# Kernel optimization log

Hardware: AMD Instinct MI355X
Metric: run time of the kernel (lower is better)

## Reference

```python
import jax, jax.numpy as jnp
import numpy as np

N = 50000  # num nodes


def _gcn_layer(x, W, b, src, dst, dinv):
    # PyG GCNConv: transform first, then normalized neighbor aggregation
    h = x @ W                                   # [N, out]
    norm = dinv[src] * dinv[dst]                # [E]
    msg = h[src] * norm[:, None]                # gather + scale, [E, out]
    agg = jax.ops.segment_sum(msg, dst, num_segments=N)
    agg = agg + h * (dinv * dinv)[:, None]      # self-loop term (weight 1)
    return agg + b


def setup_inputs() -> dict:
    key = jax.random.key(0)
    ks = jax.random.split(key, 9)
    x = jax.random.normal(ks[0], (N, 256), dtype=jnp.float32)
    edge_index = jax.random.randint(ks[1], (2, 800000), 0, N, dtype=jnp.int64)
    def lin(kw, kb, fan_in, fan_out):
        s = 1.0 / np.sqrt(fan_in)
        W = jax.random.uniform(kw, (fan_in, fan_out), jnp.float32, -s, s)
        b = jax.random.uniform(kb, (fan_out,), jnp.float32, -s, s)
        return W, b
    W0, b0 = lin(ks[2], ks[3], 256, 128)
    W1, b1 = lin(ks[4], ks[5], 128, 128)
    W2, b2 = lin(ks[6], ks[7], 128, 64)
    return {"x": x, "edge_index": edge_index,
            "W0": W0, "b0": b0, "W1": W1, "b1": b1, "W2": W2, "b2": b2}


def reference(x, edge_index, W0, b0, W1, b1, W2, b2):
    src, dst = edge_index[0], edge_index[1]
    # degree with implicit self loops (edge weights = 1)
    deg = jax.ops.segment_sum(jnp.ones_like(dst, dtype=x.dtype), dst,
                              num_segments=N) + 1.0
    dinv = jax.lax.rsqrt(deg)
    h = jax.nn.relu(_gcn_layer(x, W0, b0, src, dst, dinv))
    h = jax.nn.relu(_gcn_layer(h, W1, b1, src, dst, dinv))
    out = _gcn_layer(h, W2, b2, src, dst, dinv)  # no relu on final layer
    return out
```

## Files before the change

kernel.cpp:

```cpp
#include <hip/hip_runtime.h>

#define NNODES 50000
#define NEDGES 800000
#define CHUNK 3125

typedef __attribute__((ext_vector_type(8))) short short8;
typedef __attribute__((ext_vector_type(4))) float floatx4;
typedef __attribute__((ext_vector_type(8))) _Float16 f16x8;

__device__ __forceinline__ void async16(const void* g, void* l) {
    __builtin_amdgcn_global_load_lds(
        (const __attribute__((address_space(1))) unsigned int*)g,
        (__attribute__((address_space(3))) unsigned int*)l, 16, 0, 0);
}

__device__ __forceinline__ void split_bf16(float v, short& hi, short& lo) {
    unsigned u = __float_as_uint(v);
    unsigned hu = u & 0xffff0000u;
    hi = (short)(hu >> 16);
    float r = v - __uint_as_float(hu);
    lo = (short)(__float_as_uint(r) >> 16);
}


__global__ void k_wprep3(const float* __restrict__ W0, short* __restrict__ W0h,
                         short* __restrict__ W0l, const float* __restrict__ W1,
                         short* __restrict__ W1h, short* __restrict__ W1l,
                         const float* __restrict__ W2, short* __restrict__ W2h,
                         short* __restrict__ W2l) {
    int id = blockIdx.x * 256 + threadIdx.x;
    const float* W; short *Wh, *Wl; int K, F;
    if (id < 32768) { W = W0; Wh = W0h; Wl = W0l; K = 256; F = 128; }
    else if (id < 49152) { id -= 32768; W = W1; Wh = W1h; Wl = W1l; K = 128; F = 128; }
    else if (id < 57344) { id -= 49152; W = W2; Wh = W2h; Wl = W2l; K = 128; F = 64; }
    else return;
    int f = id / K, k = id - f * K;
    short h, l;
    split_bf16(W[(size_t)k * F + f], h, l);
    Wh[id] = h;
    Wl[id] = l;
}

__global__ void k_split(const float* __restrict__ x, short* __restrict__ xh,
                        short* __restrict__ xl, int* __restrict__ chist, int n8) {
    int i = blockIdx.x * 256 + threadIdx.x;
    if (i < 256) chist[i] = 0;
    if (i >= n8) return;
    float4 v0 = ((const float4*)x)[i * 2];
    float4 v1 = ((const float4*)x)[i * 2 + 1];
    float va[8] = {v0.x, v0.y, v0.z, v0.w, v1.x, v1.y, v1.z, v1.w};
    short8 h8, l8;
#pragma unroll
    for (int j = 0; j < 8; j++) {
        short h, l;
        split_bf16(va[j], h, l);
        h8[j] = h; l8[j] = l;
    }
    *(short8*)&xh[i * 8] = h8;
    *(short8*)&xl[i * 8] = l8;
}


__global__ __launch_bounds__(256) void k_p1(const int* __restrict__ dst,
                                            int* __restrict__ chist) {
    __shared__ int h[256];
    int t = threadIdx.x, b = blockIdx.x;
    h[t] = 0;
    __syncthreads();
    int e0 = b * CHUNK;
#pragma unroll
    for (int k = 0; k < 13; k++) {
        int o = k * 256 + t;
        if (o < CHUNK) atomicAdd(&h[dst[e0 + o] >> 8], 1);
    }
    __syncthreads();
    if (h[t]) atomicAdd(&chist[t], h[t]);
}

__global__ void k_cscan(const int* __restrict__ chist, int* __restrict__ coff,
                        int* __restrict__ ccur, int* __restrict__ rowptr) {
    __shared__ int s[256];
    int t = threadIdx.x;
    int v = chist[t];
    s[t] = v; __syncthreads();
    for (int o = 1; o < 256; o <<= 1) {
        int x = (t >= o) ? s[t - o] : 0;
        __syncthreads();
        s[t] += x;
        __syncthreads();
    }
    int excl = s[t] - v;
    coff[t] = excl;
    ccur[t] = excl;
    if (t == 0) rowptr[NNODES] = NEDGES;
}

__global__ __launch_bounds__(256) void k_p2(const int* __restrict__ src,
                                            const int* __restrict__ dst,
                                            int* ccur, unsigned* __restrict__ buck) {
    __shared__ int hist[256];
    __shared__ int base[256];
    int t = threadIdx.x, b = blockIdx.x;
    hist[t] = 0;
    __syncthreads();
    int e0 = b * CHUNK;
    int myb[13]; int myi[13]; unsigned pk[13];
#pragma unroll
    for (int k = 0; k < 13; k++) {
        int o = k * 256 + t;
        if (o < CHUNK) {
            int s = src[e0 + o], d = dst[e0 + o];
            int bin = d >> 8;
            myb[k] = bin;
            myi[k] = atomicAdd(&hist[bin], 1);
            pk[k] = (unsigned)s | ((unsigned)(d & 255) << 16);
        }
    }
    __syncthreads();
    base[t] = hist[t] ? atomicAdd(&ccur[t], hist[t]) : 0;
    __syncthreads();
#pragma unroll
    for (int k = 0; k < 13; k++) {
        int o = k * 256 + t;
        if (o < CHUNK) buck[base[myb[k]] + myi[k]] = pk[k];
    }
}

__global__ __launch_bounds__(256) void k_p3(const unsigned* __restrict__ buck,
                                            const int* __restrict__ coff,
                                            const int* __restrict__ chist,
                                            int* __restrict__ rowptr,
                                            float* __restrict__ dinv,
                                            int* __restrict__ ssrc) {
    __shared__ int h[256], ex[256], cur[256];
    int t = threadIdx.x, b = blockIdx.x;
    int s0 = coff[b], S = chist[b];
    h[t] = 0;
    __syncthreads();
    for (int i = t; i < S; i += 256)
        atomicAdd(&h[(buck[s0 + i] >> 16) & 255], 1);
    __syncthreads();
    int v = h[t];
    ex[t] = v; __syncthreads();
    for (int o = 1; o < 256; o <<= 1) {
        int x = (t >= o) ? ex[t - o] : 0;
        __syncthreads();
        ex[t] += x;
        __syncthreads();
    }
    int excl = ex[t] - v;
    int n = b * 256 + t;
    if (n < NNODES) {
        rowptr[n] = s0 + excl;
        dinv[n] = rsqrtf((float)v + 1.0f);
    }
    cur[t] = excl;
    __syncthreads();
    for (int i = t; i < S; i += 256) {
        unsigned pk = buck[s0 + i];
        int dl = (pk >> 16) & 255;
        int p = atomicAdd(&cur[dl], 1);
        ssrc[s0 + p] = (int)(pk & 0xFFFFu);
    }
}


template <int BN>
__global__ __launch_bounds__(256) void k_gemm2(
    const short* __restrict__ Ah, const short* __restrict__ Al,
    const short* __restrict__ Bh, const short* __restrict__ Bl,
    const float* __restrict__ dinv, _Float16* __restrict__ g16,
    int M, int K) {
    constexpr int BM = 64, BK = 64;
    constexpr int NT = BN / 16;
    __shared__ __align__(16) short sAh[BM * BK], sAl[BM * BK];
    __shared__ __align__(16) short sBh[BN * BK], sBl[BN * BK];

    const int tid = threadIdx.x, lane = tid & 63, w = tid >> 6;
    const int row0 = blockIdx.x * BM;
    const int lr = lane >> 3;
    const int lz = lane & 7;
    const int swz = (lz ^ lr) * 8;
    const int fr = lane & 15, fq = lane >> 4;

    floatx4 acc[NT] = {};

    for (int k0 = 0; k0 < K; k0 += BK) {
#pragma unroll
        for (int jj = 0; jj < 2; jj++) {
            int j = w * 2 + jj;
            int grow = row0 + j * 8 + lr;
            if (grow >= M) grow = M - 1;
            size_t go = (size_t)grow * K + k0 + swz;
            async16(&Ah[go], &sAh[j * 8 * BK + lane * 8]);
            async16(&Al[go], &sAl[j * 8 * BK + lane * 8]);
        }
#pragma unroll
        for (int jj = 0; jj < BN / 32; jj++) {
            int j = w * (BN / 32) + jj;
            size_t go = (size_t)(j * 8 + lr) * K + k0 + swz;
            async16(&Bh[go], &sBh[j * 8 * BK + lane * 8]);
            async16(&Bl[go], &sBl[j * 8 * BK + lane * 8]);
        }
        __syncthreads();

#pragma unroll
        for (int ks = 0; ks < 2; ks++) {
            int R = w * 16 + fr;
            int ca = ((ks * 4 + fq) ^ (R & 7)) * 8;
            short8 ah = *(const short8*)&sAh[R * BK + ca];
            short8 al = *(const short8*)&sAl[R * BK + ca];
#pragma unroll
            for (int nt = 0; nt < NT; nt++) {
                int n = nt * 16 + fr;
                int cb = ((ks * 4 + fq) ^ (n & 7)) * 8;
                short8 bh = *(const short8*)&sBh[n * BK + cb];
                short8 bl = *(const short8*)&sBl[n * BK + cb];
                acc[nt] = __builtin_amdgcn_mfma_f32_16x16x32_bf16(ah, bh, acc[nt], 0, 0, 0);
                acc[nt] = __builtin_amdgcn_mfma_f32_16x16x32_bf16(ah, bl, acc[nt], 0, 0, 0);
                acc[nt] = __builtin_amdgcn_mfma_f32_16x16x32_bf16(al, bh, acc[nt], 0, 0, 0);
            }
        }
        __syncthreads();
    }

#pragma unroll
    for (int rr = 0; rr < 4; rr++) {
        int grow = row0 + w * 16 + fq * 4 + rr;
        if (grow < M) {
            float dv = dinv[grow];
#pragma unroll
            for (int nt = 0; nt < NT; nt++)
                g16[(size_t)grow * BN + nt * 16 + fr] =
                    (_Float16)(acc[nt][rr] * dv);
        }
    }
}


__global__ __launch_bounds__(256) void k_agg(const _Float16* __restrict__ g,
                                             const int* __restrict__ ssrc,
                                             const int* __restrict__ rowptr,
                                             const float* __restrict__ dinv,
                                             const float* __restrict__ bias,
                                             float* __restrict__ outf,
                                             short* __restrict__ oh,
                                             short* __restrict__ ol,
                                             int F, int lgF8, int relu, int writebf) {
    int gid = blockIdx.x * 256 + threadIdx.x;
    int F8 = F >> 3;
    int n = gid >> lgF8;
    if (n >= NNODES) return;
    int c8 = gid & (F8 - 1);
    const f16x8* gp = (const f16x8*)g;

    f16x8 sv = gp[(size_t)n * F8 + c8];
    float a0[8], a1[8], a2[8], a3[8];
#pragma unroll
    for (int j = 0; j < 8; j++) {
        a0[j] = (float)sv[j];
        a1[j] = 0.f; a2[j] = 0.f; a3[j] = 0.f;
    }
    int e0 = rowptr[n], e1 = rowptr[n + 1];
    int e = e0;
    for (; e + 4 <= e1; e += 4) {
        int s0 = ssrc[e], s1 = ssrc[e + 1], s2 = ssrc[e + 2], s3 = ssrc[e + 3];
        f16x8 v0 = gp[(size_t)s0 * F8 + c8];
        f16x8 v1 = gp[(size_t)s1 * F8 + c8];
        f16x8 v2 = gp[(size_t)s2 * F8 + c8];
        f16x8 v3 = gp[(size_t)s3 * F8 + c8];
#pragma unroll
        for (int j = 0; j < 8; j++) {
            a0[j] += (float)v0[j];
            a1[j] += (float)v1[j];
            a2[j] += (float)v2[j];
            a3[j] += (float)v3[j];
        }
    }
    for (; e < e1; e++) {
        int s = ssrc[e];
        f16x8 v = gp[(size_t)s * F8 + c8];
#pragma unroll
        for (int j = 0; j < 8; j++) a0[j] += (float)v[j];
    }
    float dv = dinv[n];
    float o[8];
#pragma unroll
    for (int j = 0; j < 8; j++) {
        float s = (a0[j] + a1[j]) + (a2[j] + a3[j]);
        o[j] = s * dv + bias[c8 * 8 + j];
        if (relu) o[j] = fmaxf(o[j], 0.f);
    }
    if (writebf) {
        short8 h8, l8;
#pragma unroll
        for (int j = 0; j < 8; j++) {
            short h, l;
            split_bf16(o[j], h, l);
            h8[j] = h; l8[j] = l;
        }
        *(short8*)&oh[(size_t)n * F + c8 * 8] = h8;
        *(short8*)&ol[(size_t)n * F + c8 * 8] = l8;
    } else {
        *(float4*)&outf[(size_t)n * F + c8 * 8] =
            make_float4(o[0], o[1], o[2], o[3]);
        *(float4*)&outf[(size_t)n * F + c8 * 8 + 4] =
            make_float4(o[4], o[5], o[6], o[7]);
    }
}


static inline size_t align256(size_t x) { return (x + 255) & ~(size_t)255; }

extern "C" void kernel_launch(void* const* d_in, const int* in_sizes, int n_in,
                              void* d_out, int out_size, void* d_ws, size_t ws_size,
                              hipStream_t stream) {
    const float* x  = (const float*)d_in[0];
    const int*   ei = (const int*)d_in[1];
    const float* W0 = (const float*)d_in[2];
    const float* b0 = (const float*)d_in[3];
    const float* W1 = (const float*)d_in[4];
    const float* b1 = (const float*)d_in[5];
    const float* W2 = (const float*)d_in[6];
    const float* b2 = (const float*)d_in[7];
    float* out = (float*)d_out;

    const int* src = ei;
    const int* dst = ei + NEDGES;

    char* w = (char*)d_ws;
    size_t off = 0;
    float* dinv   = (float*)(w + off); off = align256(off + NNODES * 4);
    int* rowptr   = (int*)(w + off);   off = align256(off + (NNODES + 1) * 4);
    int* chist    = (int*)(w + off);   off = align256(off + 256 * 4);
    int* coff     = (int*)(w + off);   off = align256(off + 256 * 4);
    int* ccur     = (int*)(w + off);   off = align256(off + 256 * 4);
    unsigned* buck = (unsigned*)(w + off); off = align256(off + (size_t)NEDGES * 4);
    int* ssrc     = (int*)(w + off);   off = align256(off + (size_t)NEDGES * 4);
    short* W0h    = (short*)(w + off); off = align256(off + 256 * 128 * 2);
    short* W0l    = (short*)(w + off); off = align256(off + 256 * 128 * 2);
    short* W1h    = (short*)(w + off); off = align256(off + 128 * 128 * 2);
    short* W1l    = (short*)(w + off); off = align256(off + 128 * 128 * 2);
    short* W2h    = (short*)(w + off); off = align256(off + 128 * 64 * 2);
    short* W2l    = (short*)(w + off); off = align256(off + 128 * 64 * 2);
    short* xh     = (short*)(w + off); off = align256(off + (size_t)NNODES * 256 * 2);
    short* xl     = (short*)(w + off); off = align256(off + (size_t)NNODES * 256 * 2);
    short* ph     = (short*)(w + off); off = align256(off + (size_t)NNODES * 128 * 2);
    short* pl     = (short*)(w + off); off = align256(off + (size_t)NNODES * 128 * 2);
    _Float16* g16 = (_Float16*)(w + off); off = align256(off + (size_t)NNODES * 128 * 2);

    k_wprep3<<<224, 256, 0, stream>>>(W0, W0h, W0l, W1, W1h, W1l, W2, W2h, W2l);
    k_split<<<(NNODES * 32 + 255) / 256, 256, 0, stream>>>(x, xh, xl, chist,
                                                           NNODES * 32);
    k_p1<<<256, 256, 0, stream>>>(dst, chist);
    k_cscan<<<1, 256, 0, stream>>>(chist, coff, ccur, rowptr);
    k_p2<<<256, 256, 0, stream>>>(src, dst, ccur, buck);
    k_p3<<<256, 256, 0, stream>>>(buck, coff, chist, rowptr, dinv, ssrc);

    const int MB = (NNODES + 63) / 64;

    k_gemm2<128><<<MB, 256, 0, stream>>>(xh, xl, W0h, W0l, dinv, g16, NNODES, 256);
    k_agg<<<(NNODES * 16 + 255) / 256, 256, 0, stream>>>(g16, ssrc, rowptr, dinv, b0,
                                                         (float*)nullptr, ph, pl,
                                                         128, 4, 1, 1);
    k_gemm2<128><<<MB, 256, 0, stream>>>(ph, pl, W1h, W1l, dinv, g16, NNODES, 128);
    k_agg<<<(NNODES * 16 + 255) / 256, 256, 0, stream>>>(g16, ssrc, rowptr, dinv, b1,
                                                         (float*)nullptr, ph, pl,
                                                         128, 4, 1, 1);
    k_gemm2<64><<<MB, 256, 0, stream>>>(ph, pl, W2h, W2l, dinv, g16, NNODES, 128);
    k_agg<<<(NNODES * 8 + 255) / 256, 256, 0, stream>>>(g16, ssrc, rowptr, dinv, b2,
                                                        out, (short*)nullptr,
                                                        (short*)nullptr, 64, 3, 0, 0);
    (void)in_sizes; (void)n_in; (void)out_size; (void)ws_size;
}
```

Baseline: 277.2 us.

## Merge prep kernels and give each node a full wavefront for aggregation

The weight split, input split and dst histogram kernels become one launch. Each histogram block writes its own row, and the scan kernel sums those rows, replacing the global atomics and the chist zeroing. Aggregation now gives one 64-lane wavefront to each node: lanes split the edges and combine their partial sums with xor shuffles. This spreads the gather more evenly across lanes, though with about 16 edges per node many lanes sit idle, and the shuffle reduction adds overhead.

```diff
diff --git a/kernel.cpp b/kernel.cpp
--- a/kernel.cpp
+++ b/kernel.cpp
@@ -23,65 +23,69 @@
 }
 
 
-__global__ void k_wprep3(const float* __restrict__ W0, short* __restrict__ W0h,
-                         short* __restrict__ W0l, const float* __restrict__ W1,
-                         short* __restrict__ W1h, short* __restrict__ W1l,
-                         const float* __restrict__ W2, short* __restrict__ W2h,
-                         short* __restrict__ W2l) {
-    int id = blockIdx.x * 256 + threadIdx.x;
-    const float* W; short *Wh, *Wl; int K, F;
-    if (id < 32768) { W = W0; Wh = W0h; Wl = W0l; K = 256; F = 128; }
-    else if (id < 49152) { id -= 32768; W = W1; Wh = W1h; Wl = W1l; K = 128; F = 128; }
-    else if (id < 57344) { id -= 49152; W = W2; Wh = W2h; Wl = W2l; K = 128; F = 64; }
-    else return;
-    int f = id / K, k = id - f * K;
-    short h, l;
-    split_bf16(W[(size_t)k * F + f], h, l);
-    Wh[id] = h;
-    Wl[id] = l;
-}
-
-__global__ void k_split(const float* __restrict__ x, short* __restrict__ xh,
-                        short* __restrict__ xl, int* __restrict__ chist, int n8) {
-    int i = blockIdx.x * 256 + threadIdx.x;
-    if (i < 256) chist[i] = 0;
-    if (i >= n8) return;
-    float4 v0 = ((const float4*)x)[i * 2];
-    float4 v1 = ((const float4*)x)[i * 2 + 1];
-    float va[8] = {v0.x, v0.y, v0.z, v0.w, v1.x, v1.y, v1.z, v1.w};
-    short8 h8, l8;
-#pragma unroll
-    for (int j = 0; j < 8; j++) {
+#define PREP_WBLK 224
+#define PREP_SBLK 6250
+#define PREP_TOT  (PREP_WBLK + PREP_SBLK + 256)
+
+__global__ __launch_bounds__(256) void k_prep(
+    const float* __restrict__ W0, short* __restrict__ W0h, short* __restrict__ W0l,
+    const float* __restrict__ W1, short* __restrict__ W1h, short* __restrict__ W1l,
+    const float* __restrict__ W2, short* __restrict__ W2h, short* __restrict__ W2l,
+    const float* __restrict__ x, short* __restrict__ xh, short* __restrict__ xl,
+    const int* __restrict__ dst, int* __restrict__ hist2d) {
+    int b = blockIdx.x, t = threadIdx.x;
+    if (b < PREP_WBLK) {
+        int id = b * 256 + t;
+        const float* W; short *Wh, *Wl; int K;
+        if (id < 32768) { W = W0; Wh = W0h; Wl = W0l; K = 256; }
+        else if (id < 49152) { id -= 32768; W = W1; Wh = W1h; Wl = W1l; K = 128; }
+        else if (id < 57344) { id -= 49152; W = W2; Wh = W2h; Wl = W2l; K = 128; }
+        else return;
+        int F = (W == W2) ? 64 : 128;
+        int f = id / K, k = id - f * K;
         short h, l;
-        split_bf16(va[j], h, l);
-        h8[j] = h; l8[j] = l;
-    }
-    *(short8*)&xh[i * 8] = h8;
-    *(short8*)&xl[i * 8] = l8;
-}
-
-
-__global__ __launch_bounds__(256) void k_p1(const int* __restrict__ dst,
-                                            int* __restrict__ chist) {
-    __shared__ int h[256];
-    int t = threadIdx.x, b = blockIdx.x;
-    h[t] = 0;
-    __syncthreads();
-    int e0 = b * CHUNK;
-#pragma unroll
-    for (int k = 0; k < 13; k++) {
-        int o = k * 256 + t;
-        if (o < CHUNK) atomicAdd(&h[dst[e0 + o] >> 8], 1);
-    }
-    __syncthreads();
-    if (h[t]) atomicAdd(&chist[t], h[t]);
-}
-
-__global__ void k_cscan(const int* __restrict__ chist, int* __restrict__ coff,
-                        int* __restrict__ ccur, int* __restrict__ rowptr) {
+        split_bf16(W[(size_t)k * F + f], h, l);
+        Wh[id] = h;
+        Wl[id] = l;
+    } else if (b < PREP_WBLK + PREP_SBLK) {
+        int i = (b - PREP_WBLK) * 256 + t;
+        float4 v0 = ((const float4*)x)[i * 2];
+        float4 v1 = ((const float4*)x)[i * 2 + 1];
+        float va[8] = {v0.x, v0.y, v0.z, v0.w, v1.x, v1.y, v1.z, v1.w};
+        short8 h8, l8;
+#pragma unroll
+        for (int j = 0; j < 8; j++) {
+            short h, l;
+            split_bf16(va[j], h, l);
+            h8[j] = h; l8[j] = l;
+        }
+        *(short8*)&xh[i * 8] = h8;
+        *(short8*)&xl[i * 8] = l8;
+    } else {
+        __shared__ int h[256];
+        int bb = b - PREP_WBLK - PREP_SBLK;
+        h[t] = 0;
+        __syncthreads();
+        int e0 = bb * CHUNK;
+#pragma unroll
+        for (int k = 0; k < 13; k++) {
+            int o = k * 256 + t;
+            if (o < CHUNK) atomicAdd(&h[dst[e0 + o] >> 8], 1);
+        }
+        __syncthreads();
+        hist2d[bb * 256 + t] = h[t];
+    }
+}
+
+__global__ void k_cscan(const int* __restrict__ hist2d, int* __restrict__ chist,
+                        int* __restrict__ coff, int* __restrict__ ccur,
+                        int* __restrict__ rowptr) {
     __shared__ int s[256];
     int t = threadIdx.x;
-    int v = chist[t];
+    int v = 0;
+#pragma unroll 8
+    for (int b = 0; b < 256; b++) v += hist2d[b * 256 + t];
+    chist[t] = v;
     s[t] = v; __syncthreads();
     for (int o = 1; o < 256; o <<= 1) {
         int x = (t >= o) ? s[t - o] : 0;
@@ -238,74 +242,77 @@
 }
 
 
-__global__ __launch_bounds__(256) void k_agg(const _Float16* __restrict__ g,
-                                             const int* __restrict__ ssrc,
-                                             const int* __restrict__ rowptr,
-                                             const float* __restrict__ dinv,
-                                             const float* __restrict__ bias,
-                                             float* __restrict__ outf,
-                                             short* __restrict__ oh,
-                                             short* __restrict__ ol,
-                                             int F, int lgF8, int relu, int writebf) {
-    int gid = blockIdx.x * 256 + threadIdx.x;
-    int F8 = F >> 3;
-    int n = gid >> lgF8;
-    if (n >= NNODES) return;
-    int c8 = gid & (F8 - 1);
+template <int F>
+__global__ __launch_bounds__(256) void k_aggw(const _Float16* __restrict__ g,
+                                              const int* __restrict__ ssrc,
+                                              const int* __restrict__ rowptr,
+                                              const float* __restrict__ dinv,
+                                              const float* __restrict__ bias,
+                                              float* __restrict__ outf,
+                                              short* __restrict__ oh,
+                                              short* __restrict__ ol,
+                                              int relu, int writebf) {
+    constexpr int C = F / 8;
+    constexpr int S = 64 / C;
+    int wid = (blockIdx.x * 256 + threadIdx.x) >> 6;
+    if (wid >= NNODES) return;
+    int lane = threadIdx.x & 63;
+    int c = lane & (C - 1);
+    int s = lane / C;
+    int n = wid;
     const f16x8* gp = (const f16x8*)g;
 
-    f16x8 sv = gp[(size_t)n * F8 + c8];
-    float a0[8], a1[8], a2[8], a3[8];
-#pragma unroll
-    for (int j = 0; j < 8; j++) {
-        a0[j] = (float)sv[j];
-        a1[j] = 0.f; a2[j] = 0.f; a3[j] = 0.f;
-    }
+    float acc[8];
+    if (s == 0) {
+        f16x8 v = gp[(size_t)n * C + c];
+#pragma unroll
+        for (int j = 0; j < 8; j++) acc[j] = (float)v[j];
+    } else {
+#pragma unroll
+        for (int j = 0; j < 8; j++) acc[j] = 0.f;
+    }
+
     int e0 = rowptr[n], e1 = rowptr[n + 1];
-    int e = e0;
-    for (; e + 4 <= e1; e += 4) {
-        int s0 = ssrc[e], s1 = ssrc[e + 1], s2 = ssrc[e + 2], s3 = ssrc[e + 3];
-        f16x8 v0 = gp[(size_t)s0 * F8 + c8];
-        f16x8 v1 = gp[(size_t)s1 * F8 + c8];
-        f16x8 v2 = gp[(size_t)s2 * F8 + c8];
-        f16x8 v3 = gp[(size_t)s3 * F8 + c8];
+    for (int e = e0 + s; e < e1; e += S) {
+        int sn = ssrc[e];
+        f16x8 v = gp[(size_t)sn * C + c];
+#pragma unroll
+        for (int j = 0; j < 8; j++) acc[j] += (float)v[j];
+    }
+
+#pragma unroll
+    for (int m = C; m < 64; m <<= 1) {
+#pragma unroll
+        for (int j = 0; j < 8; j++) acc[j] += __shfl_xor(acc[j], m, 64);
+    }
+
+    if (s == 0) {
+        float dv = dinv[n];
+        float4 bv0 = *(const float4*)&bias[c * 8];
+        float4 bv1 = *(const float4*)&bias[c * 8 + 4];
+        float bb[8] = {bv0.x, bv0.y, bv0.z, bv0.w, bv1.x, bv1.y, bv1.z, bv1.w};
+        float o[8];
 #pragma unroll
         for (int j = 0; j < 8; j++) {
-            a0[j] += (float)v0[j];
-            a1[j] += (float)v1[j];
-            a2[j] += (float)v2[j];
-            a3[j] += (float)v3[j];
-        }
-    }
-    for (; e < e1; e++) {
-        int s = ssrc[e];
-        f16x8 v = gp[(size_t)s * F8 + c8];
-#pragma unroll
-        for (int j = 0; j < 8; j++) a0[j] += (float)v[j];
-    }
-    float dv = dinv[n];
-    float o[8];
-#pragma unroll
-    for (int j = 0; j < 8; j++) {
-        float s = (a0[j] + a1[j]) + (a2[j] + a3[j]);
-        o[j] = s * dv + bias[c8 * 8 + j];
-        if (relu) o[j] = fmaxf(o[j], 0.f);
-    }
-    if (writebf) {
-        short8 h8, l8;
-#pragma unroll
-        for (int j = 0; j < 8; j++) {
-            short h, l;
-            split_bf16(o[j], h, l);
-            h8[j] = h; l8[j] = l;
-        }
-        *(short8*)&oh[(size_t)n * F + c8 * 8] = h8;
-        *(short8*)&ol[(size_t)n * F + c8 * 8] = l8;
-    } else {
-        *(float4*)&outf[(size_t)n * F + c8 * 8] =
-            make_float4(o[0], o[1], o[2], o[3]);
-        *(float4*)&outf[(size_t)n * F + c8 * 8 + 4] =
-            make_float4(o[4], o[5], o[6], o[7]);
+            o[j] = acc[j] * dv + bb[j];
+            if (relu) o[j] = fmaxf(o[j], 0.f);
+        }
+        if (writebf) {
+            short8 h8, l8;
+#pragma unroll
+            for (int j = 0; j < 8; j++) {
+                short h, l;
+                split_bf16(o[j], h, l);
+                h8[j] = h; l8[j] = l;
+            }
+            *(short8*)&oh[(size_t)n * F + c * 8] = h8;
+            *(short8*)&ol[(size_t)n * F + c * 8] = l8;
+        } else {
+            *(float4*)&outf[(size_t)n * F + c * 8] =
+                make_float4(o[0], o[1], o[2], o[3]);
+            *(float4*)&outf[(size_t)n * F + c * 8 + 4] =
+                make_float4(o[4], o[5], o[6], o[7]);
+        }
     }
 }
 
@@ -330,46 +337,43 @@
 
     char* w = (char*)d_ws;
     size_t off = 0;
-    float* dinv   = (float*)(w + off); off = align256(off + NNODES * 4);
-    int* rowptr   = (int*)(w + off);   off = align256(off + (NNODES + 1) * 4);
-    int* chist    = (int*)(w + off);   off = align256(off + 256 * 4);
-    int* coff     = (int*)(w + off);   off = align256(off + 256 * 4);
-    int* ccur     = (int*)(w + off);   off = align256(off + 256 * 4);
+    float* dinv    = (float*)(w + off); off = align256(off + NNODES * 4);
+    int* rowptr    = (int*)(w + off);   off = align256(off + (NNODES + 1) * 4);
+    int* hist2d    = (int*)(w + off);   off = align256(off + 256 * 256 * 4);
+    int* chist     = (int*)(w + off);   off = align256(off + 256 * 4);
+    int* coff      = (int*)(w + off);   off = align256(off + 256 * 4);
+    int* ccur      = (int*)(w + off);   off = align256(off + 256 * 4);
     unsigned* buck = (unsigned*)(w + off); off = align256(off + (size_t)NEDGES * 4);
-    int* ssrc     = (int*)(w + off);   off = align256(off + (size_t)NEDGES * 4);
-    short* W0h    = (short*)(w + off); off = align256(off + 256 * 128 * 2);
-    short* W0l    = (short*)(w + off); off = align256(off + 256 * 128 * 2);
-    short* W1h    = (short*)(w + off); off = align256(off + 128 * 128 * 2);
-    short* W1l    = (short*)(w + off); off = align256(off + 128 * 128 * 2);
-    short* W2h    = (short*)(w + off); off = align256(off + 128 * 64 * 2);
-    short* W2l    = (short*)(w + off); off = align256(off + 128 * 64 * 2);
-    short* xh     = (short*)(w + off); off = align256(off + (size_t)NNODES * 256 * 2);
-    short* xl     = (short*)(w + off); off = align256(off + (size_t)NNODES * 256 * 2);
-    short* ph     = (short*)(w + off); off = align256(off + (size_t)NNODES * 128 * 2);
-    short* pl     = (short*)(w + off); off = align256(off + (size_t)NNODES * 128 * 2);
-    _Float16* g16 = (_Float16*)(w + off); off = align256(off + (size_t)NNODES * 128 * 2);
-
-    k_wprep3<<<224, 256, 0, stream>>>(W0, W0h, W0l, W1, W1h, W1l, W2, W2h, W2l);
-    k_split<<<(NNODES * 32 + 255) / 256, 256, 0, stream>>>(x, xh, xl, chist,
-                                                           NNODES * 32);
-    k_p1<<<256, 256, 0, stream>>>(dst, chist);
-    k_cscan<<<1, 256, 0, stream>>>(chist, coff, ccur, rowptr);
+    int* ssrc      = (int*)(w + off);   off = align256(off + (size_t)NEDGES * 4);
+    short* W0h     = (short*)(w + off); off = align256(off + 256 * 128 * 2);
+    short* W0l     = (short*)(w + off); off = align256(off + 256 * 128 * 2);
+    short* W1h     = (short*)(w + off); off = align256(off + 128 * 128 * 2);
+    short* W1l     = (short*)(w + off); off = align256(off + 128 * 128 * 2);
+    short* W2h     = (short*)(w + off); off = align256(off + 128 * 64 * 2);
+    short* W2l     = (short*)(w + off); off = align256(off + 128 * 64 * 2);
+    short* xh      = (short*)(w + off); off = align256(off + (size_t)NNODES * 256 * 2);
+    short* xl      = (short*)(w + off); off = align256(off + (size_t)NNODES * 256 * 2);
+    short* ph      = (short*)(w + off); off = align256(off + (size_t)NNODES * 128 * 2);
+    short* pl      = (short*)(w + off); off = align256(off + (size_t)NNODES * 128 * 2);
+    _Float16* g16  = (_Float16*)(w + off); off = align256(off + (size_t)NNODES * 128 * 2);
+
+    k_prep<<<PREP_TOT, 256, 0, stream>>>(W0, W0h, W0l, W1, W1h, W1l,
+                                         W2, W2h, W2l, x, xh, xl, dst, hist2d);
+    k_cscan<<<1, 256, 0, stream>>>(hist2d, chist, coff, ccur, rowptr);
     k_p2<<<256, 256, 0, stream>>>(src, dst, ccur, buck);
     k_p3<<<256, 256, 0, stream>>>(buck, coff, chist, rowptr, dinv, ssrc);
 
     const int MB = (NNODES + 63) / 64;
+    const int AB = (NNODES * 64 + 255) / 256;
 
     k_gemm2<128><<<MB, 256, 0, stream>>>(xh, xl, W0h, W0l, dinv, g16, NNODES, 256);
-    k_agg<<<(NNODES * 16 + 255) / 256, 256, 0, stream>>>(g16, ssrc, rowptr, dinv, b0,
-                                                         (float*)nullptr, ph, pl,
-                                                         128, 4, 1, 1);
+    k_aggw<128><<<AB, 256, 0, stream>>>(g16, ssrc, rowptr, dinv, b0,
+                                        (float*)nullptr, ph, pl, 1, 1);
     k_gemm2<128><<<MB, 256, 0, stream>>>(ph, pl, W1h, W1l, dinv, g16, NNODES, 128);
-    k_agg<<<(NNODES * 16 + 255) / 256, 256, 0, stream>>>(g16, ssrc, rowptr, dinv, b1,
-                                                         (float*)nullptr, ph, pl,
-                                                         128, 4, 1, 1);
+    k_aggw<128><<<AB, 256, 0, stream>>>(g16, ssrc, rowptr, dinv, b1,
+                                        (float*)nullptr, ph, pl, 1, 1);
     k_gemm2<64><<<MB, 256, 0, stream>>>(ph, pl, W2h, W2l, dinv, g16, NNODES, 128);
-    k_agg<<<(NNODES * 8 + 255) / 256, 256, 0, stream>>>(g16, ssrc, rowptr, dinv, b2,
-                                                        out, (short*)nullptr,
-                                                        (short*)nullptr, 64, 3, 0, 0);
+    k_aggw<64><<<AB, 256, 0, stream>>>(g16, ssrc, rowptr, dinv, b2,
+                                       out, (short*)nullptr, (short*)nullptr, 0, 0);
     (void)in_sizes; (void)n_in; (void)out_size; (void)ws_size;
 }
```

After: 300.1 us. 1.08x slower.

## Fuse CSR build into one persistent kernel with grid barriers, merge prep kernels

Applied to the files above, without the earlier changes.

Merges the weight-split and x-split kernels into a single launch, and folds the three-pass CSR construction (histogram, scan, scatter, per-bucket sort) into one 256-block kernel that synchronises with software grid barriers. The global atomic bucket allocation is replaced by a per-block 2D histogram with deterministic prefix offsets. The aggregation kernel is also templated on feature width. This removes four kernel launches and their gaps. In exchange it depends on all 256 blocks being co-resident, or the spin barrier deadlocks, and every block redundantly reads the full 256x256 histogram.

```diff
diff --git a/kernel.cpp b/kernel.cpp
--- a/kernel.cpp
+++ b/kernel.cpp
@@ -23,129 +23,129 @@
 }
 
 
-__global__ void k_wprep3(const float* __restrict__ W0, short* __restrict__ W0h,
-                         short* __restrict__ W0l, const float* __restrict__ W1,
-                         short* __restrict__ W1h, short* __restrict__ W1l,
-                         const float* __restrict__ W2, short* __restrict__ W2h,
-                         short* __restrict__ W2l) {
-    int id = blockIdx.x * 256 + threadIdx.x;
-    const float* W; short *Wh, *Wl; int K, F;
-    if (id < 32768) { W = W0; Wh = W0h; Wl = W0l; K = 256; F = 128; }
-    else if (id < 49152) { id -= 32768; W = W1; Wh = W1h; Wl = W1l; K = 128; F = 128; }
-    else if (id < 57344) { id -= 49152; W = W2; Wh = W2h; Wl = W2l; K = 128; F = 64; }
-    else return;
-    int f = id / K, k = id - f * K;
-    short h, l;
-    split_bf16(W[(size_t)k * F + f], h, l);
-    Wh[id] = h;
-    Wl[id] = l;
-}
-
-__global__ void k_split(const float* __restrict__ x, short* __restrict__ xh,
-                        short* __restrict__ xl, int* __restrict__ chist, int n8) {
-    int i = blockIdx.x * 256 + threadIdx.x;
-    if (i < 256) chist[i] = 0;
-    if (i >= n8) return;
-    float4 v0 = ((const float4*)x)[i * 2];
-    float4 v1 = ((const float4*)x)[i * 2 + 1];
-    float va[8] = {v0.x, v0.y, v0.z, v0.w, v1.x, v1.y, v1.z, v1.w};
-    short8 h8, l8;
-#pragma unroll
-    for (int j = 0; j < 8; j++) {
+#define PREP_WBLK 224
+#define PREP_SBLK 6250
+#define PREP_TOT  (PREP_WBLK + PREP_SBLK)
+
+__global__ __launch_bounds__(256) void k_prep(
+    const float* __restrict__ W0, short* __restrict__ W0h, short* __restrict__ W0l,
+    const float* __restrict__ W1, short* __restrict__ W1h, short* __restrict__ W1l,
+    const float* __restrict__ W2, short* __restrict__ W2h, short* __restrict__ W2l,
+    const float* __restrict__ x, short* __restrict__ xh, short* __restrict__ xl,
+    int* __restrict__ bar) {
+    int b = blockIdx.x, t = threadIdx.x;
+    if (b == 0 && t < 8) bar[t] = 0;
+    if (b < PREP_WBLK) {
+        int id = b * 256 + t;
+        const float* W; short *Wh, *Wl; int K, F;
+        if (id < 32768) { W = W0; Wh = W0h; Wl = W0l; K = 256; F = 128; }
+        else if (id < 49152) { id -= 32768; W = W1; Wh = W1h; Wl = W1l; K = 128; F = 128; }
+        else if (id < 57344) { id -= 49152; W = W2; Wh = W2h; Wl = W2l; K = 128; F = 64; }
+        else return;
+        int f = id / K, k = id - f * K;
         short h, l;
-        split_bf16(va[j], h, l);
-        h8[j] = h; l8[j] = l;
-    }
-    *(short8*)&xh[i * 8] = h8;
-    *(short8*)&xl[i * 8] = l8;
-}
-
-
-__global__ __launch_bounds__(256) void k_p1(const int* __restrict__ dst,
-                                            int* __restrict__ chist) {
-    __shared__ int h[256];
+        split_bf16(W[(size_t)k * F + f], h, l);
+        Wh[id] = h;
+        Wl[id] = l;
+    } else {
+        int i = (b - PREP_WBLK) * 256 + t;
+        float4 v0 = ((const float4*)x)[i * 2];
+        float4 v1 = ((const float4*)x)[i * 2 + 1];
+        float va[8] = {v0.x, v0.y, v0.z, v0.w, v1.x, v1.y, v1.z, v1.w};
+        short8 h8, l8;
+#pragma unroll
+        for (int j = 0; j < 8; j++) {
+            short h, l;
+            split_bf16(va[j], h, l);
+            h8[j] = h; l8[j] = l;
+        }
+        *(short8*)&xh[i * 8] = h8;
+        *(short8*)&xl[i * 8] = l8;
+    }
+}
+
+
+__device__ __forceinline__ void gridbar(int* bar, int idx) {
+    __syncthreads();
+    if (threadIdx.x == 0) {
+        __threadfence();
+        atomicAdd(&bar[idx], 1);
+        while (atomicAdd(&bar[idx], 0) < 256) __builtin_amdgcn_s_sleep(1);
+        __threadfence();
+    }
+    __syncthreads();
+}
+
+__global__ __launch_bounds__(256) void k_csr(const int* __restrict__ src,
+                                             const int* __restrict__ dst,
+                                             int* __restrict__ hist2d,
+                                             unsigned* __restrict__ buck,
+                                             int* __restrict__ rowptr,
+                                             float* __restrict__ dinv,
+                                             int* __restrict__ ssrc,
+                                             int* bar) {
+    __shared__ int h[256], ex[256], cur[256];
+    __shared__ int scoff[256], stot[256];
     int t = threadIdx.x, b = blockIdx.x;
+    int e0 = b * CHUNK;
+
     h[t] = 0;
     __syncthreads();
-    int e0 = b * CHUNK;
 #pragma unroll
     for (int k = 0; k < 13; k++) {
         int o = k * 256 + t;
         if (o < CHUNK) atomicAdd(&h[dst[e0 + o] >> 8], 1);
     }
     __syncthreads();
-    if (h[t]) atomicAdd(&chist[t], h[t]);
-}
-
-__global__ void k_cscan(const int* __restrict__ chist, int* __restrict__ coff,
-                        int* __restrict__ ccur, int* __restrict__ rowptr) {
-    __shared__ int s[256];
-    int t = threadIdx.x;
-    int v = chist[t];
-    s[t] = v; __syncthreads();
+    hist2d[b * 256 + t] = h[t];
+
+    gridbar(bar, 0);
+
+    int pre = 0, tot = 0;
+    for (int bb = 0; bb < 256; bb++) {
+        int v = hist2d[bb * 256 + t];
+        pre += (bb < b) ? v : 0;
+        tot += v;
+    }
+    ex[t] = tot;
+    __syncthreads();
     for (int o = 1; o < 256; o <<= 1) {
-        int x = (t >= o) ? s[t - o] : 0;
-        __syncthreads();
-        s[t] += x;
-        __syncthreads();
-    }
-    int excl = s[t] - v;
-    coff[t] = excl;
-    ccur[t] = excl;
-    if (t == 0) rowptr[NNODES] = NEDGES;
-}
-
-__global__ __launch_bounds__(256) void k_p2(const int* __restrict__ src,
-                                            const int* __restrict__ dst,
-                                            int* ccur, unsigned* __restrict__ buck) {
-    __shared__ int hist[256];
-    __shared__ int base[256];
-    int t = threadIdx.x, b = blockIdx.x;
-    hist[t] = 0;
-    __syncthreads();
-    int e0 = b * CHUNK;
-    int myb[13]; int myi[13]; unsigned pk[13];
+        int xx = (t >= o) ? ex[t - o] : 0;
+        __syncthreads();
+        ex[t] += xx;
+        __syncthreads();
+    }
+    int coff = ex[t] - tot;
+    scoff[t] = coff;
+    stot[t] = tot;
+    cur[t] = coff + pre;
+    __syncthreads();
+
 #pragma unroll
     for (int k = 0; k < 13; k++) {
         int o = k * 256 + t;
         if (o < CHUNK) {
             int s = src[e0 + o], d = dst[e0 + o];
-            int bin = d >> 8;
-            myb[k] = bin;
-            myi[k] = atomicAdd(&hist[bin], 1);
-            pk[k] = (unsigned)s | ((unsigned)(d & 255) << 16);
-        }
-    }
-    __syncthreads();
-    base[t] = hist[t] ? atomicAdd(&ccur[t], hist[t]) : 0;
-    __syncthreads();
-#pragma unroll
-    for (int k = 0; k < 13; k++) {
-        int o = k * 256 + t;
-        if (o < CHUNK) buck[base[myb[k]] + myi[k]] = pk[k];
-    }
-}
-
-__global__ __launch_bounds__(256) void k_p3(const unsigned* __restrict__ buck,
-                                            const int* __restrict__ coff,
-                                            const int* __restrict__ chist,
-                                            int* __restrict__ rowptr,
-                                            float* __restrict__ dinv,
-                                            int* __restrict__ ssrc) {
-    __shared__ int h[256], ex[256], cur[256];
-    int t = threadIdx.x, b = blockIdx.x;
-    int s0 = coff[b], S = chist[b];
+            int p = atomicAdd(&cur[d >> 8], 1);
+            buck[p] = (unsigned)s | ((unsigned)(d & 255) << 16);
+        }
+    }
+
+    gridbar(bar, 1);
+
+    int s0 = scoff[b], S = stot[b];
     h[t] = 0;
     __syncthreads();
     for (int i = t; i < S; i += 256)
         atomicAdd(&h[(buck[s0 + i] >> 16) & 255], 1);
     __syncthreads();
     int v = h[t];
-    ex[t] = v; __syncthreads();
+    ex[t] = v;
+    __syncthreads();
     for (int o = 1; o < 256; o <<= 1) {
-        int x = (t >= o) ? ex[t - o] : 0;
-        __syncthreads();
-        ex[t] += x;
+        int xx = (t >= o) ? ex[t - o] : 0;
+        __syncthreads();
+        ex[t] += xx;
         __syncthreads();
     }
     int excl = ex[t] - v;
@@ -154,6 +154,7 @@
         rowptr[n] = s0 + excl;
         dinv[n] = rsqrtf((float)v + 1.0f);
     }
+    if (b == 0 && t == 0) rowptr[NNODES] = NEDGES;
     cur[t] = excl;
     __syncthreads();
     for (int i = t; i < S; i += 256) {
@@ -238,6 +239,7 @@
 }
 
 
+template <int F>
 __global__ __launch_bounds__(256) void k_agg(const _Float16* __restrict__ g,
                                              const int* __restrict__ ssrc,
                                              const int* __restrict__ rowptr,
@@ -246,12 +248,12 @@
                                              float* __restrict__ outf,
                                              short* __restrict__ oh,
                                              short* __restrict__ ol,
-                                             int F, int lgF8, int relu, int writebf) {
+                                             int relu, int writebf) {
+    constexpr int F8 = F / 8;
     int gid = blockIdx.x * 256 + threadIdx.x;
-    int F8 = F >> 3;
-    int n = gid >> lgF8;
+    int n = gid / F8;
     if (n >= NNODES) return;
-    int c8 = gid & (F8 - 1);
+    int c8 = gid - n * F8;
     const f16x8* gp = (const f16x8*)g;
 
     f16x8 sv = gp[(size_t)n * F8 + c8];
@@ -330,46 +332,40 @@
 
     char* w = (char*)d_ws;
     size_t off = 0;
-    float* dinv   = (float*)(w + off); off = align256(off + NNODES * 4);
-    int* rowptr   = (int*)(w + off);   off = align256(off + (NNODES + 1) * 4);
-    int* chist    = (int*)(w + off);   off = align256(off + 256 * 4);
-    int* coff     = (int*)(w + off);   off = align256(off + 256 * 4);
-    int* ccur     = (int*)(w + off);   off = align256(off + 256 * 4);
+    float* dinv    = (float*)(w + off); off = align256(off + NNODES * 4);
+    int* rowptr    = (int*)(w + off);   off = align256(off + (NNODES + 1) * 4);
+    int* bar       = (int*)(w + off);   off = align256(off + 8 * 4);
+    int* hist2d    = (int*)(w + off);   off = align256(off + 256 * 256 * 4);
     unsigned* buck = (unsigned*)(w + off); off = align256(off + (size_t)NEDGES * 4);
-    int* ssrc     = (int*)(w + off);   off = align256(off + (size_t)NEDGES * 4);
-    short* W0h    = (short*)(w + off); off = align256(off + 256 * 128 * 2);
-    short* W0l    = (short*)(w + off); off = align256(off + 256 * 128 * 2);
-    short* W1h    = (short*)(w + off); off = align256(off + 128 * 128 * 2);
-    short* W1l    = (short*)(w + off); off = align256(off + 128 * 128 * 2);
-    short* W2h    = (short*)(w + off); off = align256(off + 128 * 64 * 2);
-    short* W2l    = (short*)(w + off); off = align256(off + 128 * 64 * 2);
-    short* xh     = (short*)(w + off); off = align256(off + (size_t)NNODES * 256 * 2);
-    short* xl     = (short*)(w + off); off = align256(off + (size_t)NNODES * 256 * 2);
-    short* ph     = (short*)(w + off); off = align256(off + (size_t)NNODES * 128 * 2);
-    short* pl     = (short*)(w + off); off = align256(off + (size_t)NNODES * 128 * 2);
-    _Float16* g16 = (_Float16*)(w + off); off = align256(off + (size_t)NNODES * 128 * 2);
-
-    k_wprep3<<<224, 256, 0, stream>>>(W0, W0h, W0l, W1, W1h, W1l, W2, W2h, W2l);
-    k_split<<<(NNODES * 32 + 255) / 256, 256, 0, stream>>>(x, xh, xl, chist,
-                                                           NNODES * 32);
-    k_p1<<<256, 256, 0, stream>>>(dst, chist);
-    k_cscan<<<1, 256, 0, stream>>>(chist, coff, ccur, rowptr);
-    k_p2<<<256, 256, 0, stream>>>(src, dst, ccur, buck);
-    k_p3<<<256, 256, 0, stream>>>(buck, coff, chist, rowptr, dinv, ssrc);
+    int* ssrc      = (int*)(w + off);   off = align256(off + (size_t)NEDGES * 4);
+    short* W0h     = (short*)(w + off); off = align256(off + 256 * 128 * 2);
+    short* W0l     = (short*)(w + off); off = align256(off + 256 * 128 * 2);
+    short* W1h     = (short*)(w + off); off = align256(off + 128 * 128 * 2);
+    short* W1l     = (short*)(w + off); off = align256(off + 128 * 128 * 2);
+    short* W2h     = (short*)(w + off); off = align256(off + 128 * 64 * 2);
+    short* W2l     = (short*)(w + off); off = align256(off + 128 * 64 * 2);
+    short* xh      = (short*)(w + off); off = align256(off + (size_t)NNODES * 256 * 2);
+    short* xl      = (short*)(w + off); off = align256(off + (size_t)NNODES * 256 * 2);
+    short* ph      = (short*)(w + off); off = align256(off + (size_t)NNODES * 128 * 2);
+    short* pl      = (short*)(w + off); off = align256(off + (size_t)NNODES * 128 * 2);
+    _Float16* g16  = (_Float16*)(w + off); off = align256(off + (size_t)NNODES * 128 * 2);
+
+    k_prep<<<PREP_TOT, 256, 0, stream>>>(W0, W0h, W0l, W1, W1h, W1l,
+                                         W2, W2h, W2l, x, xh, xl, bar);
+    k_csr<<<256, 256, 0, stream>>>(src, dst, hist2d, buck, rowptr, dinv, ssrc, bar);
 
     const int MB = (NNODES + 63) / 64;
+    const int AB128 = (NNODES * 16 + 255) / 256;
+    const int AB64  = (NNODES * 8 + 255) / 256;
 
     k_gemm2<128><<<MB, 256, 0, stream>>>(xh, xl, W0h, W0l, dinv, g16, NNODES, 256);
-    k_agg<<<(NNODES * 16 + 255) / 256, 256, 0, stream>>>(g16, ssrc, rowptr, dinv, b0,
-                                                         (float*)nullptr, ph, pl,
-                                                         128, 4, 1, 1);
+    k_agg<128><<<AB128, 256, 0, stream>>>(g16, ssrc, rowptr, dinv, b0,
+                                          (float*)nullptr, ph, pl, 1, 1);
     k_gemm2<128><<<MB, 256, 0, stream>>>(ph, pl, W1h, W1l, dinv, g16, NNODES, 128);
-    k_agg<<<(NNODES * 16 + 255) / 256, 256, 0, stream>>>(g16, ssrc, rowptr, dinv, b1,
-                                                         (float*)nullptr, ph, pl,
-                                                         128, 4, 1, 1);
+    k_agg<128><<<AB128, 256, 0, stream>>>(g16, ssrc, rowptr, dinv, b1,
+                                          (float*)nullptr, ph, pl, 1, 1);
     k_gemm2<64><<<MB, 256, 0, stream>>>(ph, pl, W2h, W2l, dinv, g16, NNODES, 128);
-    k_agg<<<(NNODES * 8 + 255) / 256, 256, 0, stream>>>(g16, ssrc, rowptr, dinv, b2,
-                                                        out, (short*)nullptr,
-                                                        (short*)nullptr, 64, 3, 0, 0);
+    k_agg<64><<<AB64, 256, 0, stream>>>(g16, ssrc, rowptr, dinv, b2,
+                                        out, (short*)nullptr, (short*)nullptr, 0, 0);
     (void)in_sizes; (void)n_in; (void)out_size; (void)ws_size;
 }
```

Result: slower. 318.6 us (+14.9%).
